# Optimization experiments

Measured on AMD Instinct MI355X. Metric: run time of the kernel, lower is better.

The kernel has to match this reference:

```python
import jax, jax.numpy as jnp
import numpy as np

D_MODEL = 1024
N_HEADS = 16
D_HEAD = D_MODEL // N_HEADS

def setup_inputs() -> dict:
    key = jax.random.key(0)
    kx, kq, kk, kv, ko = jax.random.split(key, 5)
    s = 1.0 / np.sqrt(D_MODEL)
    return {
        "x": jax.random.normal(kx, (4, 2048, D_MODEL), dtype=jnp.float32),
        "W_q": jax.random.normal(kq, (D_MODEL, D_MODEL), dtype=jnp.float32) * s,
        "W_k": jax.random.normal(kk, (D_MODEL, D_MODEL), dtype=jnp.float32) * s,
        "W_v": jax.random.normal(kv, (D_MODEL, D_MODEL), dtype=jnp.float32) * s,
        "W_o": jax.random.normal(ko, (D_MODEL, D_MODEL), dtype=jnp.float32) * s,
    }

def reference(x, W_q, W_k, W_v, W_o):
    B, L, _ = x.shape
    def heads(h):  # (B,L,D) -> (B,H,L,d_head)
        return h.reshape(B, L, N_HEADS, D_HEAD).transpose(0, 2, 1, 3)
    # nn.Linear: y = x @ W.T
    q = heads(x @ W_q.T)
    k = heads(x @ W_k.T)
    v = heads(x @ W_v.T)
    scores = jnp.einsum('bhqd,bhkd->bhqk', q, k) / jnp.sqrt(jnp.float32(D_HEAD))
    attn = jax.nn.softmax(scores, axis=-1)
    ctx = jnp.einsum('bhqk,bhkd->bhqd', attn, v)
    ctx = ctx.transpose(0, 2, 1, 3).reshape(B, L, D_MODEL)
    return ctx @ W_o.T
```

## Files before the change

### kernel.cpp

```cpp
#include <hip/hip_runtime.h>
#include <hip/hip_fp16.h>

typedef _Float16 f16;
typedef _Float16 f16x2 __attribute__((ext_vector_type(2)));
typedef _Float16 f16x4 __attribute__((ext_vector_type(4)));
typedef _Float16 f16x8 __attribute__((ext_vector_type(8)));
typedef float f32x4 __attribute__((ext_vector_type(4)));
typedef float f32x16 __attribute__((ext_vector_type(16)));

#define NHEADS 16
#define DHEAD 64
#define DM 1024
#define BATCH 4
#define SEQ 2048
#define MTOT (BATCH*SEQ)

__device__ inline void gload_lds16(const void* g, void* l) {
  __builtin_amdgcn_global_load_lds(
      (const __attribute__((address_space(1))) void*)g,
      (__attribute__((address_space(3))) void*)l, 16, 0, 0);
}

__device__ inline float max3f(float a, float b, float c) {
  return fmaxf(fmaxf(a, b), c);
}

__device__ inline unsigned pkrtz(float a, float b) {
  auto h = __builtin_amdgcn_cvt_pkrtz(a, b);
  unsigned u; __builtin_memcpy(&u, &h, 4); return u;
}

__device__ inline float accum2(unsigned w, float acc) {
  f16x2 p; __builtin_memcpy(&p, &w, 4);
#if __has_builtin(__builtin_amdgcn_fdot2)
  const f16x2 one2 = {(f16)1, (f16)1};
  return __builtin_amdgcn_fdot2(p, one2, acc, false);
#else
  return acc + (float)p[0] + (float)p[1];
#endif
}

__global__ __launch_bounds__(256) void cvt_f32_f16_k(const float* __restrict__ s,
                                                     f16* __restrict__ d, int n) {
  int i = (blockIdx.x * 256 + threadIdx.x) * 8;
  if (i + 8 <= n) {
    float4 a = *reinterpret_cast<const float4*>(s + i);
    float4 b = *reinterpret_cast<const float4*>(s + i + 4);
    f16x8 h = {(f16)a.x,(f16)a.y,(f16)a.z,(f16)a.w,(f16)b.x,(f16)b.y,(f16)b.z,(f16)b.w};
    *reinterpret_cast<f16x8*>(d + i) = h;
  } else {
    for (int j = i; j < n; ++j) d[j] = (f16)s[j];
  }
}

__global__ __launch_bounds__(256) void cvt_w4_k(const float* __restrict__ w0,
                                                const float* __restrict__ w1,
                                                const float* __restrict__ w2,
                                                const float* __restrict__ w3,
                                                f16* __restrict__ d) {
  int which = blockIdx.x >> 9;
  const float* s = which == 0 ? w0 : which == 1 ? w1 : which == 2 ? w2 : w3;
  int off = ((blockIdx.x & 511) * 256 + threadIdx.x) * 8;
  float4 a = *reinterpret_cast<const float4*>(s + off);
  float4 b = *reinterpret_cast<const float4*>(s + off + 4);
  f16x8 h = {(f16)a.x,(f16)a.y,(f16)a.z,(f16)a.w,(f16)b.x,(f16)b.y,(f16)b.z,(f16)b.w};
  *reinterpret_cast<f16x8*>(d + (size_t)which * DM * DM + off) = h;
}

template <int MODE>
__device__ void gemm_nt_body(const f16* __restrict__ A, const f16* __restrict__ Bw,
                             void* __restrict__ outp, int n0, float oscale,
                             f16* Ah, f16* Bh) {
  const int tx = threadIdx.x;
  const int wave = tx >> 6, lane = tx & 63;
  const int m0 = blockIdx.y * 128;
  const int wm = (wave >> 1) * 64, wn = (wave & 1) * 64;

  f32x4 acc[4][4];
#pragma unroll
  for (int i = 0; i < 4; ++i)
#pragma unroll
    for (int j = 0; j < 4; ++j) acc[i][j] = {0.f, 0.f, 0.f, 0.f};

  const int srow = lane >> 2;
  const int scol = (lane & 3) * 8;

  auto stage = [&](int buf, int k0) {
#pragma unroll
    for (int i = 0; i < 2; ++i) {
      int chunk = wave * 2 + i;
      gload_lds16(A  + (size_t)(m0 + chunk * 16 + srow) * DM + k0 + scol,
                  Ah + buf * 4096 + chunk * 512);
      gload_lds16(Bw + (size_t)(n0 + chunk * 16 + srow) * DM + k0 + scol,
                  Bh + buf * 4096 + chunk * 512);
    }
  };

  stage(0, 0);
  __syncthreads();
  for (int k0 = 0; k0 < DM; k0 += 32) {
    const int cur = (k0 >> 5) & 1;
    if (k0 + 32 < DM) stage(cur ^ 1, k0 + 32);

    const f16* Ac = Ah + cur * 4096;
    const f16* Bc = Bh + cur * 4096;
    f16x8 af[4], bf[4];
#pragma unroll
    for (int i = 0; i < 4; ++i)
      af[i] = *reinterpret_cast<const f16x8*>(Ac + (wm + i * 16 + (lane & 15)) * 32 + (lane >> 4) * 8);
#pragma unroll
    for (int j = 0; j < 4; ++j)
      bf[j] = *reinterpret_cast<const f16x8*>(Bc + (wn + j * 16 + (lane & 15)) * 32 + (lane >> 4) * 8);
#pragma unroll
    for (int i = 0; i < 4; ++i)
#pragma unroll
      for (int j = 0; j < 4; ++j)
        acc[i][j] = __builtin_amdgcn_mfma_f32_16x16x32_f16(af[i], bf[j], acc[i][j], 0, 0, 0);
    __syncthreads();
  }

  const int r0 = (lane >> 4) * 4, c0 = lane & 15;
#pragma unroll
  for (int i = 0; i < 4; ++i)
#pragma unroll
    for (int j = 0; j < 4; ++j)
#pragma unroll
      for (int r = 0; r < 4; ++r) {
        int gm = m0 + wm + i * 16 + r0 + r;
        int gn = n0 + wn + j * 16 + c0;
        float v = acc[i][j][r] * oscale;
        if (MODE == 2) {
          ((float*)outp)[(size_t)gm * DM + gn] = v;
        } else {
          int b = gm >> 11, l = gm & 2047, h = gn >> 6, d = gn & 63;
          size_t idx = (MODE == 0)
            ? (((size_t)(b * NHEADS + h) * SEQ + l) * DHEAD + d)
            : (((size_t)(b * NHEADS + h) * DHEAD + d) * SEQ + l);
          ((f16*)outp)[idx] = (f16)v;
        }
      }
}

__global__ __launch_bounds__(256) void gemm_qkv(const f16* __restrict__ xh,
                                                const f16* __restrict__ Wf,
                                                f16* __restrict__ Qb,
                                                f16* __restrict__ Kb,
                                                f16* __restrict__ VTb,
                                                float qscale) {
  __shared__ f16 Ah[2 * 128 * 32];
  __shared__ f16 Bh[2 * 128 * 32];
  int which = blockIdx.x >> 3;
  int n0 = (blockIdx.x & 7) * 128;
  const f16* Bw = Wf + (size_t)which * DM * DM;
  if (which == 0)      gemm_nt_body<0>(xh, Bw, Qb,  n0, qscale, Ah, Bh);
  else if (which == 1) gemm_nt_body<0>(xh, Bw, Kb,  n0, 1.0f,  Ah, Bh);
  else                 gemm_nt_body<1>(xh, Bw, VTb, n0, 1.0f,  Ah, Bh);
}

__global__ __launch_bounds__(256) void gemm_out(const f16* __restrict__ A,
                                                const f16* __restrict__ Bw,
                                                float* __restrict__ outp) {
  __shared__ f16 Ah[2 * 128 * 32];
  __shared__ f16 Bh[2 * 128 * 32];
  gemm_nt_body<2>(A, Bw, outp, blockIdx.x * 128, 1.0f, Ah, Bh);
}

__global__ __launch_bounds__(256, 4) void attn_k(const f16* __restrict__ Q,
                                                 const f16* __restrict__ Kg,
                                                 const f16* __restrict__ VT,
                                                 f16* __restrict__ ctx) {
  __shared__ f16 Kt[2][64 * 64];
  __shared__ f16 Vt[2][64 * 64];
  const int tx = threadIdx.x, wave = tx >> 6, lane = tx & 63;
  const int m = lane & 31, hi = lane >> 5, m7 = m & 7;

  const int bid = blockIdx.y * 16 + blockIdx.x;
  const int swz = (bid & 7) * 128 + (bid >> 3);
  const int bh = swz >> 4;
  const int q0 = (swz & 15) * 128;

  const f16* Qb = Q  + (size_t)bh * SEQ * DHEAD;
  const f16* Kb = Kg + (size_t)bh * SEQ * DHEAD;
  const f16* Vb = VT + (size_t)bh * DHEAD * SEQ;

  const int gi0 = wave * 128 + lane, gi1 = gi0 + 64;
  const int r0s = gi0 >> 3, sc0 = (((gi0 & 7) ^ (r0s & 7))) * 8;
  const int r1s = gi1 >> 3, sc1 = (((gi1 & 7) ^ (r1s & 7))) * 8;

  auto stage = [&](int buf, int k0) {
    gload_lds16(Kb + (size_t)(k0 + r0s) * DHEAD + sc0, &Kt[buf][(size_t)(wave * 128) * 8]);
    gload_lds16(Kb + (size_t)(k0 + r1s) * DHEAD + sc1, &Kt[buf][(size_t)(wave * 128 + 64) * 8]);
    gload_lds16(Vb + (size_t)r0s * SEQ + k0 + sc0,     &Vt[buf][(size_t)(wave * 128) * 8]);
    gload_lds16(Vb + (size_t)r1s * SEQ + k0 + sc1,     &Vt[buf][(size_t)(wave * 128 + 64) * 8]);
  };

  f16x8 qb[4];
#pragma unroll
  for (int s = 0; s < 4; ++s)
    qb[s] = *reinterpret_cast<const f16x8*>(
        Qb + (size_t)(q0 + wave * 32 + m) * DHEAD + s * 16 + hi * 8);

  f32x16 oacc[2];
#pragma unroll
  for (int r = 0; r < 16; ++r) { oacc[0][r] = 0.f; oacc[1][r] = 0.f; }
  float lsum = 0.f;
  float mrun = -1e30f;

  auto compute = [&](const f16* Kc, const f16* Vc) {
#pragma unroll
    for (int kt = 0; kt < 2; ++kt) {
      f32x16 st;
#pragma unroll
      for (int r = 0; r < 16; ++r) st[r] = 0.f;
      __builtin_amdgcn_s_setprio(1);
#pragma unroll
      for (int s = 0; s < 4; ++s) {
        f16x8 ka = *reinterpret_cast<const f16x8*>(
            Kc + ((kt * 32 + m) * 8 + ((2 * s + hi) ^ m7)) * 8);
        st = __builtin_amdgcn_mfma_f32_32x32x16_f16(ka, qb[s], st, 0, 0, 0);
      }
      __builtin_amdgcn_s_setprio(0);

      float a0 = max3f(st[0], st[1], st[2]);
      float a1 = max3f(st[3], st[4], st[5]);
      float a2 = max3f(st[6], st[7], st[8]);
      float a3 = max3f(st[9], st[10], st[11]);
      float a4 = max3f(st[12], st[13], st[14]);
      float mx = fmaxf(fmaxf(max3f(a0, a1, a2), fmaxf(a3, a4)), st[15]);
      mx = fmaxf(mx, __shfl_xor(mx, 32));

      if (!__all(mx <= mrun + 8.f)) {
        float mnew = fmaxf(mrun, mx);
        float scl = __builtin_amdgcn_exp2f(mrun - mnew);
#pragma unroll
        for (int r = 0; r < 16; ++r) { oacc[0][r] *= scl; oacc[1][r] *= scl; }
        lsum *= scl;
        mrun = mnew;
      }

      unsigned pk[8];
#pragma unroll
      for (int j = 0; j < 8; ++j)
        pk[j] = pkrtz(__builtin_amdgcn_exp2f(st[2 * j] - mrun),
                      __builtin_amdgcn_exp2f(st[2 * j + 1] - mrun));
#pragma unroll
      for (int j = 0; j < 8; ++j) lsum = accum2(pk[j], lsum);

      __builtin_amdgcn_s_setprio(1);
#pragma unroll
      for (int c1 = 0; c1 < 2; ++c1) {
        const int c = kt * 2 + c1;
        unsigned w0 = pk[4 * c1 + 0], w1 = pk[4 * c1 + 1];
        unsigned w2 = pk[4 * c1 + 2], w3 = pk[4 * c1 + 3];
        asm("v_permlane32_swap_b32 %0, %1" : "+v"(w0), "+v"(w2));
        asm("v_permlane32_swap_b32 %0, %1" : "+v"(w1), "+v"(w3));
        union { unsigned u[4]; f16x8 h; } pu;
        pu.u[0] = w0; pu.u[1] = w1; pu.u[2] = w2; pu.u[3] = w3;
#pragma unroll
        for (int dt = 0; dt < 2; ++dt) {
          f16x8 va = *reinterpret_cast<const f16x8*>(
              Vc + ((dt * 32 + m) * 8 + ((2 * c + hi) ^ m7)) * 8);
          oacc[dt] = __builtin_amdgcn_mfma_f32_32x32x16_f16(va, pu.h, oacc[dt], 0, 0, 0);
        }
      }
      __builtin_amdgcn_s_setprio(0);
    }
  };

  stage(0, 0);
  __syncthreads();
  for (int tt = 0; tt < 32; tt += 2) {
    stage(1, (tt + 1) * 64);
    compute(Kt[0], Vt[0]);
    __syncthreads();
    if (tt + 2 < 32) stage(0, (tt + 2) * 64);
    compute(Kt[1], Vt[1]);
    __syncthreads();
  }

  const float ltot = lsum + __shfl_xor(lsum, 32);
  const float inv = 1.0f / ltot;
  const int b = bh >> 4, hd = bh & 15;
  const int q = q0 + wave * 32 + m;
  f16* obase = ctx + ((size_t)b * SEQ + q) * DM + hd * DHEAD;
#pragma unroll
  for (int dt = 0; dt < 2; ++dt)
#pragma unroll
    for (int t = 0; t < 4; ++t) {
      f16x4 o = {(f16)(oacc[dt][4 * t + 0] * inv), (f16)(oacc[dt][4 * t + 1] * inv),
                 (f16)(oacc[dt][4 * t + 2] * inv), (f16)(oacc[dt][4 * t + 3] * inv)};
      *reinterpret_cast<f16x4*>(obase + dt * 32 + t * 8 + 4 * hi) = o;
    }
}

extern "C" void kernel_launch(void* const* d_in, const int* in_sizes, int n_in,
                              void* d_out, int out_size, void* d_ws, size_t ws_size,
                              hipStream_t stream) {
  (void)in_sizes; (void)n_in; (void)out_size; (void)ws_size;
  const float* x  = (const float*)d_in[0];
  const float* Wq = (const float*)d_in[1];
  const float* Wk = (const float*)d_in[2];
  const float* Wv = (const float*)d_in[3];
  const float* Wo = (const float*)d_in[4];

  char* ws = (char*)d_ws;
  const size_t SZ_X = (size_t)MTOT * DM * sizeof(f16);
  const size_t SZ_W = (size_t)DM * DM * sizeof(f16);
  f16* xh  = (f16*)(ws);
  f16* wfh = (f16*)(ws + SZ_X);
  f16* woh = (f16*)(ws + SZ_X + 3 * SZ_W);
  f16* Qb  = (f16*)(ws + 1 * SZ_X + 4 * SZ_W);
  f16* Kb  = (f16*)(ws + 2 * SZ_X + 4 * SZ_W);
  f16* VTb = (f16*)(ws + 3 * SZ_X + 4 * SZ_W);
  f16* ctx = xh;

  const int nx = MTOT * DM;
  const float QSCALE = 0.125f * 1.44269504088896f;

  cvt_f32_f16_k<<<nx / 2048, 256, 0, stream>>>(x, xh, nx);
  cvt_w4_k<<<2048, 256, 0, stream>>>(Wq, Wk, Wv, Wo, wfh);

  gemm_qkv<<<dim3(24, MTOT / 128), 256, 0, stream>>>(xh, wfh, Qb, Kb, VTb, QSCALE);

  attn_k<<<dim3(SEQ / 128, BATCH * NHEADS), 256, 0, stream>>>(Qb, Kb, VTb, ctx);

  gemm_out<<<dim3(DM / 128, MTOT / 128), 256, 0, stream>>>(ctx, woh, (float*)d_out);
}
```

Baseline: 205.3 us.

## Use 256-row 8-wave GEMM tiles with triple-buffered swizzled LDS and 512-thread attention

Rewrites the projection GEMMs to use 512-thread blocks with 256x256 (QKV) or 256x128 (output) tiles, a three-stage LDS ring driven by explicit vmcnt waits and raw barriers, an XOR-swizzled LDS layout, and setprio around MFMA bursts. Attention blocks grow to 8 waves covering 256 queries, so each K/V tile staged in LDS is shared by twice as many waves. The goal is more data reuse per global load, fewer LDS bank conflicts and better overlap of loads with MFMA work. The cost is higher register pressure, fewer blocks in the grid and tighter dependence on hand-counted vmcnt values.

```diff
diff --git a/kernel.cpp b/kernel.cpp
--- a/kernel.cpp
+++ b/kernel.cpp
@@ -67,67 +67,95 @@
   *reinterpret_cast<f16x8*>(d + (size_t)which * DM * DM + off) = h;
 }
 
-template <int MODE>
-__device__ void gemm_nt_body(const f16* __restrict__ A, const f16* __restrict__ Bw,
-                             void* __restrict__ outp, int n0, float oscale,
-                             f16* Ah, f16* Bh) {
+template <int MODE, int BN>
+__device__ void gemm8_body(const f16* __restrict__ A, const f16* __restrict__ Bw,
+                           void* __restrict__ outp, int n0, float oscale,
+                           f16* Ah, f16* Bh) {
   const int tx = threadIdx.x;
   const int wave = tx >> 6, lane = tx & 63;
-  const int m0 = blockIdx.y * 128;
-  const int wm = (wave >> 1) * 64, wn = (wave & 1) * 64;
-
-  f32x4 acc[4][4];
-#pragma unroll
-  for (int i = 0; i < 4; ++i)
-#pragma unroll
-    for (int j = 0; j < 4; ++j) acc[i][j] = {0.f, 0.f, 0.f, 0.f};
-
-  const int srow = lane >> 2;
-  const int scol = (lane & 3) * 8;
+  const int m0 = blockIdx.y * 256;
+  const int wm = wave >> 2, wn = wave & 3;
+  constexpr int NF = BN / 64;
+
+  f32x4 acc[8][NF];
+#pragma unroll
+  for (int i = 0; i < 8; ++i)
+#pragma unroll
+    for (int j = 0; j < NF; ++j) acc[i][j] = {0.f, 0.f, 0.f, 0.f};
+
+  const int srA = tx >> 2;
+  const int gsw = ((tx & 3) ^ ((tx >> 3) & 3)) * 8;
+  const int rl = lane & 15;
+  const int gr = ((lane >> 4) ^ ((rl >> 1) & 3)) * 8;
 
   auto stage = [&](int buf, int k0) {
-#pragma unroll
-    for (int i = 0; i < 2; ++i) {
-      int chunk = wave * 2 + i;
-      gload_lds16(A  + (size_t)(m0 + chunk * 16 + srow) * DM + k0 + scol,
-                  Ah + buf * 4096 + chunk * 512);
-      gload_lds16(Bw + (size_t)(n0 + chunk * 16 + srow) * DM + k0 + scol,
-                  Bh + buf * 4096 + chunk * 512);
+    const f16* Ag = A + (size_t)(m0 + srA) * DM + k0 + gsw;
+    f16* Ad = Ah + buf * 8192;
+    gload_lds16(Ag,                     Ad + (wave * 64) * 8);
+    gload_lds16(Ag + (size_t)128 * DM,  Ad + (512 + wave * 64) * 8);
+    const f16* Bg = Bw + (size_t)(n0 + srA) * DM + k0 + gsw;
+    f16* Bd = Bh + buf * (BN * 32);
+    if constexpr (BN == 256) {
+      gload_lds16(Bg,                     Bd + (wave * 64) * 8);
+      gload_lds16(Bg + (size_t)128 * DM,  Bd + (512 + wave * 64) * 8);
+    } else {
+      gload_lds16(Bg, Bd + (wave * 64) * 8);
     }
   };
 
   stage(0, 0);
-  __syncthreads();
-  for (int k0 = 0; k0 < DM; k0 += 32) {
-    const int cur = (k0 >> 5) & 1;
-    if (k0 + 32 < DM) stage(cur ^ 1, k0 + 32);
-
-    const f16* Ac = Ah + cur * 4096;
-    const f16* Bc = Bh + cur * 4096;
-    f16x8 af[4], bf[4];
+  stage(1, 32);
+  int cur = 0;
+  for (int t = 0; t < 32; ++t) {
+    if (t == 31) {
+      asm volatile("s_waitcnt vmcnt(0)" ::: "memory");
+    } else if constexpr (BN == 256) {
+      asm volatile("s_waitcnt vmcnt(4)" ::: "memory");
+    } else {
+      asm volatile("s_waitcnt vmcnt(3)" ::: "memory");
+    }
+    __builtin_amdgcn_s_barrier();
+    if (t < 30) stage(cur == 0 ? 2 : cur - 1, (t + 2) * 32);
+
+    const f16* Ac = Ah + cur * 8192;
+    const f16* Bc = Bh + cur * (BN * 32);
+    f16x8 av[4], bv[NF];
 #pragma unroll
     for (int i = 0; i < 4; ++i)
-      af[i] = *reinterpret_cast<const f16x8*>(Ac + (wm + i * 16 + (lane & 15)) * 32 + (lane >> 4) * 8);
-#pragma unroll
-    for (int j = 0; j < 4; ++j)
-      bf[j] = *reinterpret_cast<const f16x8*>(Bc + (wn + j * 16 + (lane & 15)) * 32 + (lane >> 4) * 8);
+      av[i] = *reinterpret_cast<const f16x8*>(Ac + (wm * 128 + i * 16 + rl) * 32 + gr);
+#pragma unroll
+    for (int j = 0; j < NF; ++j)
+      bv[j] = *reinterpret_cast<const f16x8*>(Bc + (wn * (BN / 4) + j * 16 + rl) * 32 + gr);
+    __builtin_amdgcn_s_setprio(1);
 #pragma unroll
     for (int i = 0; i < 4; ++i)
 #pragma unroll
-      for (int j = 0; j < 4; ++j)
-        acc[i][j] = __builtin_amdgcn_mfma_f32_16x16x32_f16(af[i], bf[j], acc[i][j], 0, 0, 0);
-    __syncthreads();
+      for (int j = 0; j < NF; ++j)
+        acc[i][j] = __builtin_amdgcn_mfma_f32_16x16x32_f16(av[i], bv[j], acc[i][j], 0, 0, 0);
+    __builtin_amdgcn_s_setprio(0);
+    __builtin_amdgcn_s_barrier();
+#pragma unroll
+    for (int i = 0; i < 4; ++i)
+      av[i] = *reinterpret_cast<const f16x8*>(Ac + (wm * 128 + 64 + i * 16 + rl) * 32 + gr);
+    __builtin_amdgcn_s_setprio(1);
+#pragma unroll
+    for (int i = 0; i < 4; ++i)
+#pragma unroll
+      for (int j = 0; j < NF; ++j)
+        acc[4 + i][j] = __builtin_amdgcn_mfma_f32_16x16x32_f16(av[i], bv[j], acc[4 + i][j], 0, 0, 0);
+    __builtin_amdgcn_s_setprio(0);
+    cur = cur == 2 ? 0 : cur + 1;
   }
 
-  const int r0 = (lane >> 4) * 4, c0 = lane & 15;
-#pragma unroll
-  for (int i = 0; i < 4; ++i)
-#pragma unroll
-    for (int j = 0; j < 4; ++j)
+  const int r0 = (lane >> 4) * 4;
+#pragma unroll
+  for (int i = 0; i < 8; ++i)
+#pragma unroll
+    for (int j = 0; j < NF; ++j)
 #pragma unroll
       for (int r = 0; r < 4; ++r) {
-        int gm = m0 + wm + i * 16 + r0 + r;
-        int gn = n0 + wn + j * 16 + c0;
+        int gm = m0 + wm * 128 + i * 16 + r0 + r;
+        int gn = n0 + wn * (BN / 4) + j * 16 + rl;
         float v = acc[i][j][r] * oscale;
         if (MODE == 2) {
           ((float*)outp)[(size_t)gm * DM + gn] = v;
@@ -141,31 +169,31 @@
       }
 }
 
-__global__ __launch_bounds__(256) void gemm_qkv(const f16* __restrict__ xh,
-                                                const f16* __restrict__ Wf,
-                                                f16* __restrict__ Qb,
-                                                f16* __restrict__ Kb,
-                                                f16* __restrict__ VTb,
-                                                float qscale) {
-  __shared__ f16 Ah[2 * 128 * 32];
-  __shared__ f16 Bh[2 * 128 * 32];
-  int which = blockIdx.x >> 3;
-  int n0 = (blockIdx.x & 7) * 128;
+__global__ __launch_bounds__(512, 2) void gemm_qkv(const f16* __restrict__ xh,
+                                                   const f16* __restrict__ Wf,
+                                                   f16* __restrict__ Qb,
+                                                   f16* __restrict__ Kb,
+                                                   f16* __restrict__ VTb,
+                                                   float qscale) {
+  __shared__ f16 Ah[3 * 8192];
+  __shared__ f16 Bh[3 * 8192];
+  int which = blockIdx.x >> 2;
+  int n0 = (blockIdx.x & 3) * 256;
   const f16* Bw = Wf + (size_t)which * DM * DM;
-  if (which == 0)      gemm_nt_body<0>(xh, Bw, Qb,  n0, qscale, Ah, Bh);
-  else if (which == 1) gemm_nt_body<0>(xh, Bw, Kb,  n0, 1.0f,  Ah, Bh);
-  else                 gemm_nt_body<1>(xh, Bw, VTb, n0, 1.0f,  Ah, Bh);
-}
-
-__global__ __launch_bounds__(256) void gemm_out(const f16* __restrict__ A,
-                                                const f16* __restrict__ Bw,
-                                                float* __restrict__ outp) {
-  __shared__ f16 Ah[2 * 128 * 32];
-  __shared__ f16 Bh[2 * 128 * 32];
-  gemm_nt_body<2>(A, Bw, outp, blockIdx.x * 128, 1.0f, Ah, Bh);
-}
-
-__global__ __launch_bounds__(256, 4) void attn_k(const f16* __restrict__ Q,
+  if (which == 0)      gemm8_body<0, 256>(xh, Bw, Qb,  n0, qscale, Ah, Bh);
+  else if (which == 1) gemm8_body<0, 256>(xh, Bw, Kb,  n0, 1.0f,  Ah, Bh);
+  else                 gemm8_body<1, 256>(xh, Bw, VTb, n0, 1.0f,  Ah, Bh);
+}
+
+__global__ __launch_bounds__(512, 2) void gemm_out(const f16* __restrict__ A,
+                                                   const f16* __restrict__ Bw,
+                                                   float* __restrict__ outp) {
+  __shared__ f16 Ah[3 * 8192];
+  __shared__ f16 Bh[3 * 4096];
+  gemm8_body<2, 128>(A, Bw, outp, blockIdx.x * 128, 1.0f, Ah, Bh);
+}
+
+__global__ __launch_bounds__(512, 4) void attn_k(const f16* __restrict__ Q,
                                                  const f16* __restrict__ Kg,
                                                  const f16* __restrict__ VT,
                                                  f16* __restrict__ ctx) {
@@ -174,24 +202,21 @@
   const int tx = threadIdx.x, wave = tx >> 6, lane = tx & 63;
   const int m = lane & 31, hi = lane >> 5, m7 = m & 7;
 
-  const int bid = blockIdx.y * 16 + blockIdx.x;
-  const int swz = (bid & 7) * 128 + (bid >> 3);
-  const int bh = swz >> 4;
-  const int q0 = (swz & 15) * 128;
+  const int bid = blockIdx.y * 8 + blockIdx.x;
+  const int swz = (bid & 7) * 64 + (bid >> 3);
+  const int bh = swz >> 3;
+  const int q0 = (swz & 7) * 256;
 
   const f16* Qb = Q  + (size_t)bh * SEQ * DHEAD;
   const f16* Kb = Kg + (size_t)bh * SEQ * DHEAD;
   const f16* Vb = VT + (size_t)bh * DHEAD * SEQ;
 
-  const int gi0 = wave * 128 + lane, gi1 = gi0 + 64;
-  const int r0s = gi0 >> 3, sc0 = (((gi0 & 7) ^ (r0s & 7))) * 8;
-  const int r1s = gi1 >> 3, sc1 = (((gi1 & 7) ^ (r1s & 7))) * 8;
+  const int rs = tx >> 3;
+  const int sc = ((tx & 7) ^ (rs & 7)) * 8;
 
   auto stage = [&](int buf, int k0) {
-    gload_lds16(Kb + (size_t)(k0 + r0s) * DHEAD + sc0, &Kt[buf][(size_t)(wave * 128) * 8]);
-    gload_lds16(Kb + (size_t)(k0 + r1s) * DHEAD + sc1, &Kt[buf][(size_t)(wave * 128 + 64) * 8]);
-    gload_lds16(Vb + (size_t)r0s * SEQ + k0 + sc0,     &Vt[buf][(size_t)(wave * 128) * 8]);
-    gload_lds16(Vb + (size_t)r1s * SEQ + k0 + sc1,     &Vt[buf][(size_t)(wave * 128 + 64) * 8]);
+    gload_lds16(Kb + (size_t)(k0 + rs) * DHEAD + sc, &Kt[buf][(size_t)(wave * 64) * 8]);
+    gload_lds16(Vb + (size_t)rs * SEQ + k0 + sc,     &Vt[buf][(size_t)(wave * 64) * 8]);
   };
 
   f16x8 qb[4];
@@ -320,9 +345,9 @@
   cvt_f32_f16_k<<<nx / 2048, 256, 0, stream>>>(x, xh, nx);
   cvt_w4_k<<<2048, 256, 0, stream>>>(Wq, Wk, Wv, Wo, wfh);
 
-  gemm_qkv<<<dim3(24, MTOT / 128), 256, 0, stream>>>(xh, wfh, Qb, Kb, VTb, QSCALE);
-
-  attn_k<<<dim3(SEQ / 128, BATCH * NHEADS), 256, 0, stream>>>(Qb, Kb, VTb, ctx);
-
-  gemm_out<<<dim3(DM / 128, MTOT / 128), 256, 0, stream>>>(ctx, woh, (float*)d_out);
-}
+  gemm_qkv<<<dim3(12, MTOT / 256), 512, 0, stream>>>(xh, wfh, Qb, Kb, VTb, QSCALE);
+
+  attn_k<<<dim3(SEQ / 256, BATCH * NHEADS), 512, 0, stream>>>(Qb, Kb, VTb, ctx);
+
+  gemm_out<<<dim3(DM / 128, MTOT / 256), 512, 0, stream>>>(ctx, woh, (float*)d_out);
+}
```

Result: slower. 219.2 us (+6.8%).

## Enlarge attention blocks to 8 waves and swizzle GEMM block order

Applied to the files above, without the earlier changes.

The attention kernel now uses 512 threads and covers 256 queries per block. Each K/V tile staged in LDS is therefore shared by twice as many query rows, and each thread issues half as many staging loads. Both GEMM kernels remap their linear block id with an XCD-style swizzle so that neighbouring blocks share A/B tiles in cache. The risks are lower occupancy from the larger blocks (launch bounds 512,4) and fewer attention blocks (512) to fill the CUs.

```diff
diff --git a/kernel.cpp b/kernel.cpp
--- a/kernel.cpp
+++ b/kernel.cpp
@@ -69,11 +69,10 @@
 
 template <int MODE>
 __device__ void gemm_nt_body(const f16* __restrict__ A, const f16* __restrict__ Bw,
-                             void* __restrict__ outp, int n0, float oscale,
+                             void* __restrict__ outp, int m0, int n0, float oscale,
                              f16* Ah, f16* Bh) {
   const int tx = threadIdx.x;
   const int wave = tx >> 6, lane = tx & 63;
-  const int m0 = blockIdx.y * 128;
   const int wm = (wave >> 1) * 64, wn = (wave & 1) * 64;
 
   f32x4 acc[4][4];
@@ -149,12 +148,16 @@
                                                 float qscale) {
   __shared__ f16 Ah[2 * 128 * 32];
   __shared__ f16 Bh[2 * 128 * 32];
-  int which = blockIdx.x >> 3;
-  int n0 = (blockIdx.x & 7) * 128;
+  const int p = blockIdx.y * 24 + blockIdx.x;
+  const int sw = (p & 7) * 192 + (p >> 3);
+  const int yy = sw / 24, xx = sw - yy * 24;
+  const int which = xx >> 3;
+  const int n0 = (xx & 7) * 128;
+  const int m0 = yy * 128;
   const f16* Bw = Wf + (size_t)which * DM * DM;
-  if (which == 0)      gemm_nt_body<0>(xh, Bw, Qb,  n0, qscale, Ah, Bh);
-  else if (which == 1) gemm_nt_body<0>(xh, Bw, Kb,  n0, 1.0f,  Ah, Bh);
-  else                 gemm_nt_body<1>(xh, Bw, VTb, n0, 1.0f,  Ah, Bh);
+  if (which == 0)      gemm_nt_body<0>(xh, Bw, Qb,  m0, n0, qscale, Ah, Bh);
+  else if (which == 1) gemm_nt_body<0>(xh, Bw, Kb,  m0, n0, 1.0f,  Ah, Bh);
+  else                 gemm_nt_body<1>(xh, Bw, VTb, m0, n0, 1.0f,  Ah, Bh);
 }
 
 __global__ __launch_bounds__(256) void gemm_out(const f16* __restrict__ A,
@@ -162,10 +165,13 @@
                                                 float* __restrict__ outp) {
   __shared__ f16 Ah[2 * 128 * 32];
   __shared__ f16 Bh[2 * 128 * 32];
-  gemm_nt_body<2>(A, Bw, outp, blockIdx.x * 128, 1.0f, Ah, Bh);
-}
-
-__global__ __launch_bounds__(256, 4) void attn_k(const f16* __restrict__ Q,
+  const int p = blockIdx.y * 8 + blockIdx.x;
+  const int sw = (p & 7) * 64 + (p >> 3);
+  const int yy = sw >> 3, xx = sw & 7;
+  gemm_nt_body<2>(A, Bw, outp, yy * 128, xx * 128, 1.0f, Ah, Bh);
+}
+
+__global__ __launch_bounds__(512, 4) void attn_k(const f16* __restrict__ Q,
                                                  const f16* __restrict__ Kg,
                                                  const f16* __restrict__ VT,
                                                  f16* __restrict__ ctx) {
@@ -174,24 +180,21 @@
   const int tx = threadIdx.x, wave = tx >> 6, lane = tx & 63;
   const int m = lane & 31, hi = lane >> 5, m7 = m & 7;
 
-  const int bid = blockIdx.y * 16 + blockIdx.x;
-  const int swz = (bid & 7) * 128 + (bid >> 3);
-  const int bh = swz >> 4;
-  const int q0 = (swz & 15) * 128;
+  const int bid = blockIdx.y * 8 + blockIdx.x;
+  const int swz = (bid & 7) * 64 + (bid >> 3);
+  const int bh = swz >> 3;
+  const int q0 = (swz & 7) * 256;
 
   const f16* Qb = Q  + (size_t)bh * SEQ * DHEAD;
   const f16* Kb = Kg + (size_t)bh * SEQ * DHEAD;
   const f16* Vb = VT + (size_t)bh * DHEAD * SEQ;
 
-  const int gi0 = wave * 128 + lane, gi1 = gi0 + 64;
-  const int r0s = gi0 >> 3, sc0 = (((gi0 & 7) ^ (r0s & 7))) * 8;
-  const int r1s = gi1 >> 3, sc1 = (((gi1 & 7) ^ (r1s & 7))) * 8;
+  const int rs = tx >> 3;
+  const int sc = ((tx & 7) ^ (rs & 7)) * 8;
 
   auto stage = [&](int buf, int k0) {
-    gload_lds16(Kb + (size_t)(k0 + r0s) * DHEAD + sc0, &Kt[buf][(size_t)(wave * 128) * 8]);
-    gload_lds16(Kb + (size_t)(k0 + r1s) * DHEAD + sc1, &Kt[buf][(size_t)(wave * 128 + 64) * 8]);
-    gload_lds16(Vb + (size_t)r0s * SEQ + k0 + sc0,     &Vt[buf][(size_t)(wave * 128) * 8]);
-    gload_lds16(Vb + (size_t)r1s * SEQ + k0 + sc1,     &Vt[buf][(size_t)(wave * 128 + 64) * 8]);
+    gload_lds16(Kb + (size_t)(k0 + rs) * DHEAD + sc, &Kt[buf][(size_t)(wave * 64) * 8]);
+    gload_lds16(Vb + (size_t)rs * SEQ + k0 + sc,     &Vt[buf][(size_t)(wave * 64) * 8]);
   };
 
   f16x8 qb[4];
@@ -322,7 +325,7 @@
 
   gemm_qkv<<<dim3(24, MTOT / 128), 256, 0, stream>>>(xh, wfh, Qb, Kb, VTb, QSCALE);
 
-  attn_k<<<dim3(SEQ / 128, BATCH * NHEADS), 256, 0, stream>>>(Qb, Kb, VTb, ctx);
+  attn_k<<<dim3(SEQ / 256, BATCH * NHEADS), 512, 0, stream>>>(Qb, Kb, VTb, ctx);
 
   gemm_out<<<dim3(DM / 128, MTOT / 128), 256, 0, stream>>>(ctx, woh, (float*)d_out);
 }
```

Result: slower. 223.0 us (+8.7%).
